# Kernel tuning notes

Hardware: AMD Instinct MI355X
Metric: run time of the kernel (lower is better)

Reference implementation:

```python
import jax, jax.numpy as jnp
import numpy as np

NUM_HEAD = 8
EPS = 1e-12  # matches torch F.normalize default eps


def setup_inputs() -> dict:
    key = jax.random.key(0)
    k1, k2, k3 = jax.random.split(key, 3)
    B, N, C = 8, 8192, 384
    x = jax.random.normal(k1, (B, N, C), dtype=jnp.float32)
    # torch Linear weights: (out_features, in_features)
    w_qkv = jax.random.normal(k2, (3 * C, C), dtype=jnp.float32) * (C ** -0.5)
    w_proj = jax.random.normal(k3, (C, C), dtype=jnp.float32) * (C ** -0.5)
    b_proj = jnp.zeros((C,), dtype=jnp.float32)
    return {"x": x, "w_qkv": w_qkv, "w_proj": w_proj, "b_proj": b_proj}


def _l2norm(t):
    # F.normalize(t, dim=-1): t / max(||t||_2, eps)
    n = jnp.sqrt(jnp.sum(t * t, axis=-1, keepdims=True))
    return t / jnp.maximum(n, EPS)


def reference(x, w_qkv, w_proj, b_proj):
    B, N, C = x.shape
    H = NUM_HEAD
    Dh = C // H
    qkv = x @ w_qkv.T  # (B, N, 3C), qkv_bias=False
    qkv = qkv.reshape(B, N, 3, H, Dh).transpose(2, 0, 3, 1, 4)  # (3, B, H, N, Dh)
    q, k, v = qkv[0], qkv[1], qkv[2]
    # transpose(-2, -1) -> (B, H, Dh, N); normalize along N (cross-covariance attn)
    q = _l2norm(jnp.swapaxes(q, -2, -1))
    k = _l2norm(jnp.swapaxes(k, -2, -1))
    v = jnp.swapaxes(v, -2, -1)  # (B, H, Dh, N)
    attn = jnp.einsum('bhdn,bhen->bhde', q, k)  # (B, H, Dh, Dh)
    attn = jax.nn.softmax(attn, axis=-1)
    out = jnp.einsum('bhde,bhen->bhdn', attn, v)  # (B, H, Dh, N)
    out = out.transpose(0, 3, 1, 2).reshape(B, N, C)  # (B, N, C)
    out = out @ w_proj.T + b_proj
    return out
```

## Files before the change

### kernel.cpp

```cpp
#include <hip/hip_runtime.h>
#include <hip/hip_bf16.h>
#include <stdint.h>


typedef __bf16 bf16_t;
typedef __attribute__((ext_vector_type(8))) __bf16 bf16x8;
typedef __attribute__((ext_vector_type(4))) __bf16 bf16x4;
typedef __attribute__((ext_vector_type(4))) float f32x4;

#define NTOK 8192
#define CDIM 384
#define WH   25165824
#define DHN  393216

#define XCHUNKS 3145728
#define TCHUNKS 3201024

__device__ __forceinline__ f32x4 mfma16(bf16x8 a, bf16x8 b, f32x4 c) {
  return __builtin_amdgcn_mfma_f32_16x16x32_bf16(a, b, c, 0, 0, 0);
}

__device__ __forceinline__ void gload16(bf16_t* lds, const bf16_t* g) {
  __builtin_amdgcn_global_load_lds(
      (const __attribute__((address_space(1))) void*)g,
      (__attribute__((address_space(3))) void*)lds, 16, 0, 0);
}

template <bool BF16>
__device__ __forceinline__ bf16x8 load8(const void* p, int idx) {
  if constexpr (BF16) {
    return *(const bf16x8*)((const bf16_t*)p + idx);
  } else {
    const float* f = (const float*)p + idx;
    f32x4 a = *(const f32x4*)f;
    f32x4 b = *(const f32x4*)(f + 4);
    bf16x8 r;
    r[0] = (bf16_t)a[0]; r[1] = (bf16_t)a[1]; r[2] = (bf16_t)a[2]; r[3] = (bf16_t)a[3];
    r[4] = (bf16_t)b[0]; r[5] = (bf16_t)b[1]; r[6] = (bf16_t)b[2]; r[7] = (bf16_t)b[3];
    return r;
  }
}

__global__ void k_probe(const uint32_t* __restrict__ X, int* __restrict__ flag) {
  __shared__ int cnt;
  if (threadIdx.x == 0) cnt = 0;
  __syncthreads();
  const uint32_t w = X[threadIdx.x];
  const int e = (int)((w >> 7) & 0xFF);
  const int sane = (e >= 110 && e <= 131) ? 1 : 0;
  atomicAdd(&cnt, sane);
  __syncthreads();
  if (threadIdx.x == 0) *flag = (cnt >= 128) ? 1 : 0;
}

__global__ void k_zero(float* __restrict__ p, int n) {
  int i = blockIdx.x * 256 + threadIdx.x;
  if (i < n) p[i] = 0.f;
}

__global__ void k_cvt(const void* __restrict__ X, const void* __restrict__ Wqkv,
                      bf16_t* __restrict__ Xf, bf16_t* __restrict__ Wf,
                      const int* __restrict__ flagp) {
  const int isb = *flagp;
  const int G = gridDim.x * 256;
  for (int c = blockIdx.x * 256 + threadIdx.x; c < TCHUNKS; c += G) {
    const bool isX = c < XCHUNKS;
    const int lc = isX ? c : c - XCHUNKS;
    const int t = lc >> 6, ln = lc & 63;
    const int tm = t / 12, tk = t - tm * 12;
    const int m = tm * 16 + (ln & 15);
    const int k = tk * 32 + ((ln >> 4) << 3);
    const int off = m * CDIM + k;
    const void* src = isX ? X : Wqkv;
    bf16_t* dst = (isX ? Xf : Wf) + (size_t)lc * 8;
    if (isb) {
      *(bf16x8*)dst = *(const bf16x8*)((const bf16_t*)src + off);
    } else {
      const float* f = (const float*)src + off;
      const f32x4 a = *(const f32x4*)f;
      const f32x4 b = *(const f32x4*)(f + 4);
      bf16x8 r;
      r[0] = (bf16_t)a[0]; r[1] = (bf16_t)a[1]; r[2] = (bf16_t)a[2]; r[3] = (bf16_t)a[3];
      r[4] = (bf16_t)b[0]; r[5] = (bf16_t)b[1]; r[6] = (bf16_t)b[2]; r[7] = (bf16_t)b[3];
      *(bf16x8*)dst = r;
    }
  }
}

__global__ __launch_bounds__(256, 3) void k_gemm_qkv(
    const bf16_t* __restrict__ Xf, const bf16_t* __restrict__ Wf,
    bf16_t* __restrict__ qkv) {
  __shared__ __align__(16) bf16_t Bs[24576];

  const int tid = threadIdx.x;
  const int lane = tid & 63;
  const int wv = tid >> 6;
  const int q4 = lane >> 4, l16 = lane & 15;
  const int tok0 = blockIdx.x * 64;
  const int bb = tok0 >> 13;
  const int nB = tok0 & 8191;

  const bf16_t* Bsrc = Xf + (size_t)tok0 * CDIM;
#pragma unroll
  for (int s = 0; s < 12; s++) {
    const int chunk = s * 256 + tid;
    gload16(Bs + chunk * 8, Bsrc + chunk * 8);
  }
  __syncthreads();

  for (int jt = 0; jt < 9; jt++) {
    const int which = jt / 3;
    const int jtt = jt - which * 3;
    f32x4 acc[2][4];
#pragma unroll
    for (int i = 0; i < 2; i++)
#pragma unroll
      for (int j = 0; j < 4; j++) acc[i][j] = (f32x4){0.f, 0.f, 0.f, 0.f};

    const int rt0 = jt * 8 + wv * 2;
#pragma unroll 2
    for (int kc = 0; kc < 12; kc++) {
      bf16x8 af[2], bfr[4];
#pragma unroll
      for (int i = 0; i < 2; i++)
        af[i] = *(const bf16x8*)(Wf + (size_t)((rt0 + i) * 12 + kc) * 512 + lane * 8);
#pragma unroll
      for (int j = 0; j < 4; j++)
        bfr[j] = *(const bf16x8*)&Bs[(j * 12 + kc) * 512 + lane * 8];
      if (which < 2) {
#pragma unroll
        for (int i = 0; i < 2; i++)
#pragma unroll
          for (int j = 0; j < 4; j++) acc[i][j] = mfma16(bfr[j], af[i], acc[i][j]);
      } else {
#pragma unroll
        for (int i = 0; i < 2; i++)
#pragma unroll
          for (int j = 0; j < 4; j++) acc[i][j] = mfma16(af[i], bfr[j], acc[i][j]);
      }
    }

    if (which < 2) {
#pragma unroll
      for (int i = 0; i < 2; i++) {
        const int rin = jtt * 128 + wv * 32 + i * 16 + l16;
        const int h = rin / 48, dh = rin - h * 48;
        bf16_t* rowp = qkv + which * WH + (bb * 8 + h) * DHN + dh * NTOK
                       + nB + q4 * 4;
#pragma unroll
        for (int j = 0; j < 4; j++) {
          bf16x4 o = {(bf16_t)acc[i][j][0], (bf16_t)acc[i][j][1],
                      (bf16_t)acc[i][j][2], (bf16_t)acc[i][j][3]};
          *(bf16x4*)(rowp + j * 16) = o;
        }
      }
    } else {
#pragma unroll
      for (int i = 0; i < 2; i++) {
        const int c0 = jtt * 128 + wv * 32 + i * 16 + q4 * 4;
#pragma unroll
        for (int j = 0; j < 4; j++) {
          const int mg = tok0 + j * 16 + l16;
          bf16x4 o = {(bf16_t)acc[i][j][0], (bf16_t)acc[i][j][1],
                      (bf16_t)acc[i][j][2], (bf16_t)acc[i][j][3]};
          *(bf16x4*)(qkv + 2 * WH + (size_t)mg * CDIM + c0) = o;
        }
      }
    }
  }
}

template <bool BF16>
__device__ __forceinline__ void qkv_body_legacy(const void* __restrict__ X,
                                                const void* __restrict__ Wqkv,
                                                bf16_t* __restrict__ qkv,
                                                bf16_t* As, bf16_t* Bs) {
  const int tid = threadIdx.x;
  const int lane = tid & 63;
  const int wr = tid >> 7, wc = (tid >> 6) & 1;
  const int q4 = lane >> 4, l16 = lane & 15;
  const int rowB0 = blockIdx.x * 128;
  const int r0 = tid >> 2, kk = (tid & 3) << 3;
  const int bb = rowB0 >> 13;
  const int nB = rowB0 & 8191;

  for (int jt = 0; jt < 9; jt++) {
    const int rowA0 = jt * 128;
    const int which = jt / 3;
    const int jtt = jt - which * 3;
    f32x4 acc[4][4];
#pragma unroll
    for (int i = 0; i < 4; i++)
#pragma unroll
      for (int j = 0; j < 4; j++) acc[i][j] = (f32x4){0.f, 0.f, 0.f, 0.f};

    for (int k0 = 0; k0 < CDIM; k0 += 32) {
      bf16x8 a0 = load8<BF16>(Wqkv, (rowA0 + r0) * CDIM + k0 + kk);
      bf16x8 a1 = load8<BF16>(Wqkv, (rowA0 + r0 + 64) * CDIM + k0 + kk);
      bf16x8 b0 = load8<BF16>(X, (rowB0 + r0) * CDIM + k0 + kk);
      bf16x8 b1 = load8<BF16>(X, (rowB0 + r0 + 64) * CDIM + k0 + kk);
      __syncthreads();
      *(bf16x8*)&As[tid * 8] = a0;
      *(bf16x8*)&As[(tid + 256) * 8] = a1;
      *(bf16x8*)&Bs[tid * 8] = b0;
      *(bf16x8*)&Bs[(tid + 256) * 8] = b1;
      __syncthreads();
      bf16x8 af[4], bfr[4];
#pragma unroll
      for (int i = 0; i < 4; i++) {
        af[i]  = *(const bf16x8*)&As[(wr * 64 + i * 16 + l16) * 32 + q4 * 8];
        bfr[i] = *(const bf16x8*)&Bs[(wc * 64 + i * 16 + l16) * 32 + q4 * 8];
      }
      if (which < 2) {
#pragma unroll
        for (int i = 0; i < 4; i++)
#pragma unroll
          for (int j = 0; j < 4; j++) acc[i][j] = mfma16(bfr[j], af[i], acc[i][j]);
      } else {
#pragma unroll
        for (int i = 0; i < 4; i++)
#pragma unroll
          for (int j = 0; j < 4; j++) acc[i][j] = mfma16(af[i], bfr[j], acc[i][j]);
      }
    }

    if (which < 2) {
#pragma unroll
      for (int i = 0; i < 4; i++) {
        const int rin = jtt * 128 + wr * 64 + i * 16 + l16;
        const int h = rin / 48, dh = rin - h * 48;
        bf16_t* rowp = qkv + which * WH + (bb * 8 + h) * DHN + dh * NTOK
                       + nB + wc * 64 + q4 * 4;
#pragma unroll
        for (int j = 0; j < 4; j++) {
          bf16x4 o = {(bf16_t)acc[i][j][0], (bf16_t)acc[i][j][1],
                      (bf16_t)acc[i][j][2], (bf16_t)acc[i][j][3]};
          *(bf16x4*)(rowp + j * 16) = o;
        }
      }
    } else {
#pragma unroll
      for (int i = 0; i < 4; i++) {
        const int rin0 = jtt * 128 + wr * 64 + i * 16 + q4 * 4;
#pragma unroll
        for (int j = 0; j < 4; j++) {
          const int mg = rowB0 + wc * 64 + j * 16 + l16;
          bf16x4 o = {(bf16_t)acc[i][j][0], (bf16_t)acc[i][j][1],
                      (bf16_t)acc[i][j][2], (bf16_t)acc[i][j][3]};
          *(bf16x4*)(qkv + 2 * WH + mg * CDIM + rin0) = o;
        }
      }
    }
  }
}

__global__ __launch_bounds__(256, 2) void k_gemm_qkv_bf16(
    const void* __restrict__ X, const void* __restrict__ Wqkv,
    bf16_t* __restrict__ qkv, const int* __restrict__ flagp) {
  __shared__ __align__(16) bf16_t As[128 * 32];
  __shared__ __align__(16) bf16_t Bs[128 * 32];
  if (!*flagp) return;
  qkv_body_legacy<true>(X, Wqkv, qkv, As, Bs);
}

__global__ __launch_bounds__(256, 2) void k_gemm_qkv_f32(
    const void* __restrict__ X, const void* __restrict__ Wqkv,
    bf16_t* __restrict__ qkv, const int* __restrict__ flagp) {
  __shared__ __align__(16) bf16_t As[128 * 32];
  __shared__ __align__(16) bf16_t Bs[128 * 32];
  if (*flagp) return;
  qkv_body_legacy<false>(X, Wqkv, qkv, As, Bs);
}

__global__ __launch_bounds__(256, 2) void k_gram(
    const bf16_t* __restrict__ qkv, float* __restrict__ S_acc, float* __restrict__ ssq_acc) {
  __shared__ __align__(16) float sm[9312];
  bf16_t* Qs = (bf16_t*)sm;
  bf16_t* Ks = Qs + 6144;
  float* ssq_sm = sm + 9216;

  const int tid = threadIdx.x;
  const int wave = tid >> 6, lane = tid & 63, q4 = lane >> 4, l16 = lane & 15;
  const int s = blockIdx.x, bh = blockIdx.y;
  const bf16_t* Qg = qkv + bh * DHN;
  const bf16_t* Kg = qkv + WH + bh * DHN;

  if (tid < 96) ssq_sm[tid] = 0.f;

  f32x4 acc[3][3];
#pragma unroll
  for (int i = 0; i < 3; i++)
#pragma unroll
    for (int j = 0; j < 3; j++) acc[i][j] = (f32x4){0.f, 0.f, 0.f, 0.f};
  float qss[3] = {0.f, 0.f, 0.f}, kss[3] = {0.f, 0.f, 0.f};

  for (int t0 = 0; t0 < 8; t0++) {
    const int n0 = s * 1024 + t0 * 128;
    bf16x8 qv[3], kv[3];
#pragma unroll
    for (int jj = 0; jj < 3; jj++) {
      const int c = jj * 256 + tid;
      const int st = c / 192, rem = c - st * 192;
      const int row = rem >> 2, kk = (rem & 3) << 3;
      const int gofs = row * NTOK + n0 + st * 32 + kk;
      qv[jj] = *(const bf16x8*)(Qg + gofs);
      kv[jj] = *(const bf16x8*)(Kg + gofs);
    }
    __syncthreads();
#pragma unroll
    for (int jj = 0; jj < 3; jj++) {
      *(bf16x8*)&Qs[(jj * 256 + tid) * 8] = qv[jj];
      *(bf16x8*)&Ks[(jj * 256 + tid) * 8] = kv[jj];
    }
    __syncthreads();
    bf16x8 qf[3], kf[3];
#pragma unroll
    for (int i = 0; i < 3; i++) {
      qf[i] = *(const bf16x8*)&Qs[wave * 1536 + (i * 16 + l16) * 32 + q4 * 8];
      kf[i] = *(const bf16x8*)&Ks[wave * 1536 + (i * 16 + l16) * 32 + q4 * 8];
    }
#pragma unroll
    for (int i = 0; i < 3; i++) {
#pragma unroll
      for (int u = 0; u < 8; u++) {
        const float qv2 = (float)qf[i][u], kv2 = (float)kf[i][u];
        qss[i] += qv2 * qv2;
        kss[i] += kv2 * kv2;
      }
#pragma unroll
      for (int j = 0; j < 3; j++) acc[i][j] = mfma16(qf[i], kf[j], acc[i][j]);
    }
  }

  __syncthreads();
  float* red = sm;
#pragma unroll
  for (int i = 0; i < 3; i++)
#pragma unroll
    for (int j = 0; j < 3; j++)
#pragma unroll
      for (int r = 0; r < 4; r++)
        red[wave * 2304 + (i * 3 + j) * 256 + lane * 4 + r] = acc[i][j][r];
#pragma unroll
  for (int i = 0; i < 3; i++) {
    atomicAdd(&ssq_sm[i * 16 + l16], qss[i]);
    atomicAdd(&ssq_sm[48 + i * 16 + l16], kss[i]);
  }
  __syncthreads();
  for (int idx = tid; idx < 2304; idx += 256) {
    const float v = red[idx] + red[2304 + idx] + red[4608 + idx] + red[6912 + idx];
    const int tile = idx >> 8, ln = (idx >> 2) & 63, r = idx & 3;
    const int i = tile / 3, j = tile - i * 3;
    const int d = i * 16 + ((ln >> 4) << 2) + r;
    const int e = j * 16 + (ln & 15);
    atomicAdd(&S_acc[bh * 2304 + d * 48 + e], v);
  }
  if (tid < 96) atomicAdd(&ssq_acc[bh * 96 + tid], ssq_sm[tid]);
}

__global__ void k_softmax(const float* __restrict__ S_acc, const float* __restrict__ ssq_acc,
                          float* __restrict__ attn_f) {
  __shared__ float invk_sm[48];
  const int bh = blockIdx.x, d = threadIdx.x;
  if (d < 48) invk_sm[d] = 1.f / fmaxf(sqrtf(ssq_acc[bh * 96 + 48 + d]), 1e-12f);
  __syncthreads();
  if (d < 48) {
    const float invq = 1.f / fmaxf(sqrtf(ssq_acc[bh * 96 + d]), 1e-12f);
    float lg[48], mx = -1e30f;
#pragma unroll
    for (int e = 0; e < 48; e++) {
      lg[e] = S_acc[bh * 2304 + d * 48 + e] * invq * invk_sm[e];
      mx = fmaxf(mx, lg[e]);
    }
    float ssum = 0.f;
#pragma unroll
    for (int e = 0; e < 48; e++) { lg[e] = expf(lg[e] - mx); ssum += lg[e]; }
    const float inv = 1.f / ssum;
#pragma unroll
    for (int e = 0; e < 48; e++) attn_f[bh * 2304 + d * 48 + e] = lg[e] * inv;
  }
}

__global__ void k_weff(
    const float* __restrict__ attn_f, const void* __restrict__ Wp,
    bf16_t* __restrict__ Weff, const int* __restrict__ flagp) {
  __shared__ float a_sm[2304];
  __shared__ float w_sm[2304];
  const int isb = *flagp;
  const int bid = blockIdx.x;
  const int ct = bid & 7, h = (bid >> 3) & 7, b = bid >> 6;
  const int bh = b * 8 + h;
  const int tid = threadIdx.x;

  for (int i = tid; i < 2304; i += 256) {
    a_sm[i] = attn_f[bh * 2304 + i];
    const int r = i / 48, c = i - r * 48;
    const int gi = (ct * 48 + r) * CDIM + h * 48 + c;
    w_sm[i] = isb ? (float)((const bf16_t*)Wp)[gi] : ((const float*)Wp)[gi];
  }
  __syncthreads();

  for (int o = tid; o < 2304; o += 256) {
    const int r = o / 48, e = o - r * 48;
    float s = 0.f;
#pragma unroll 8
    for (int d = 0; d < 48; d++) s += w_sm[r * 48 + d] * a_sm[d * 48 + e];
    Weff[b * 147456 + (ct * 48 + r) * CDIM + h * 48 + e] = (bf16_t)s;
  }
}

__global__ __launch_bounds__(256, 2) void k_gemm_out(
    const bf16_t* __restrict__ Weff, const bf16_t* __restrict__ qkv,
    const void* __restrict__ bias, void* __restrict__ out, const int* __restrict__ flagp) {
  __shared__ __align__(16) bf16_t As[2 * 4096];
  __shared__ __align__(16) bf16_t Bs[2 * 4096];
  const int isb = *flagp;
  const int tid = threadIdx.x;
  const int lane = tid & 63;
  const int wr = tid >> 7, wc = (tid >> 6) & 1;
  const int q4 = lane >> 4, l16 = lane & 15;
  const int b = blockIdx.y;
  const int rowB0 = blockIdx.x * 128;
  const bf16_t* Aa = Weff + b * 147456;
  const bf16_t* Ba = qkv + 2 * WH + b * (NTOK * CDIM);
  const int r0 = tid >> 2, kk = (tid & 3) << 3;

  auto STAGE = [&](int cts, int ks, int nxt) {
    const int rowA0 = cts * 128;
    const int k0 = ks * 32;
    bf16_t* Ad = As + nxt * 4096;
    bf16_t* Bd = Bs + nxt * 4096;
    gload16(Ad + tid * 8,         Aa + (rowA0 + r0) * CDIM + k0 + kk);
    gload16(Ad + (tid + 256) * 8, Aa + (rowA0 + r0 + 64) * CDIM + k0 + kk);
    gload16(Bd + tid * 8,         Ba + (rowB0 + r0) * CDIM + k0 + kk);
    gload16(Bd + (tid + 256) * 8, Ba + (rowB0 + r0 + 64) * CDIM + k0 + kk);
  };

  STAGE(0, 0, 0);
  __syncthreads();
  int cur = 0;

  for (int ct = 0; ct < 3; ct++) {
    const int rowA0 = ct * 128;
    f32x4 acc[4][4];
#pragma unroll
    for (int i = 0; i < 4; i++)
#pragma unroll
      for (int j = 0; j < 4; j++) acc[i][j] = (f32x4){0.f, 0.f, 0.f, 0.f};

    for (int k = 0; k < 12; k++) {
      if (!(ct == 2 && k == 11)) {
        int kn = k + 1, cn = ct;
        if (kn == 12) { kn = 0; cn = ct + 1; }
        STAGE(cn, kn, cur ^ 1);
      }
      const bf16_t* Ac = As + cur * 4096;
      const bf16_t* Bc = Bs + cur * 4096;
      bf16x8 af[4], bfr[4];
#pragma unroll
      for (int i = 0; i < 4; i++) {
        af[i]  = *(const bf16x8*)&Ac[(wr * 64 + i * 16 + l16) * 32 + q4 * 8];
        bfr[i] = *(const bf16x8*)&Bc[(wc * 64 + i * 16 + l16) * 32 + q4 * 8];
      }
#pragma unroll
      for (int i = 0; i < 4; i++)
#pragma unroll
        for (int j = 0; j < 4; j++) acc[i][j] = mfma16(af[i], bfr[j], acc[i][j]);
      __syncthreads();
      cur ^= 1;
    }

#pragma unroll
    for (int i = 0; i < 4; i++) {
      const int cg = rowA0 + wr * 64 + i * 16 + q4 * 4;
      float bv[4];
#pragma unroll
      for (int r = 0; r < 4; r++)
        bv[r] = isb ? (float)((const bf16_t*)bias)[cg + r] : ((const float*)bias)[cg + r];
#pragma unroll
      for (int j = 0; j < 4; j++) {
        const int ng = rowB0 + wc * 64 + j * 16 + l16;
        const int oi = (b * NTOK + ng) * CDIM + cg;
        if (isb) {
          bf16x4 o = {(bf16_t)(acc[i][j][0] + bv[0]), (bf16_t)(acc[i][j][1] + bv[1]),
                      (bf16_t)(acc[i][j][2] + bv[2]), (bf16_t)(acc[i][j][3] + bv[3])};
          *(bf16x4*)((bf16_t*)out + oi) = o;
        } else {
          f32x4 o = {acc[i][j][0] + bv[0], acc[i][j][1] + bv[1],
                     acc[i][j][2] + bv[2], acc[i][j][3] + bv[3]};
          *(f32x4*)((float*)out + oi) = o;
        }
      }
    }
  }
}

extern "C" void kernel_launch(void* const* d_in, const int* in_sizes, int n_in,
                              void* d_out, int out_size, void* d_ws, size_t ws_size,
                              hipStream_t stream) {
  (void)in_sizes; (void)n_in; (void)out_size;
  const void* X    = d_in[0];
  const void* Wqkv = d_in[1];
  const void* Wp   = d_in[2];
  const void* bias = d_in[3];

  char* ws = (char*)d_ws;
  bf16_t* qkv    = (bf16_t*)ws;
  float*  S_acc  = (float*)(ws + 150994944);
  float*  ssq    = (float*)(ws + 151584768);
  float*  attn_f = (float*)(ws + 151609344);
  bf16_t* Weff   = (bf16_t*)(ws + 152199168);
  int*    flag   = (int*)(ws + 154558464);
  bf16_t* Xf     = (bf16_t*)(ws + 154558720);
  bf16_t* Wf     = (bf16_t*)(ws + 204890368);

  const bool have_cvt_ws = ws_size >= 205775104ULL;

  k_probe<<<dim3(1), 256, 0, stream>>>((const uint32_t*)X, flag);
  k_zero<<<dim3(600), 256, 0, stream>>>(S_acc, 153600);
  if (have_cvt_ws) {
    k_cvt<<<dim3(2048), 256, 0, stream>>>(X, Wqkv, Xf, Wf, flag);
    k_gemm_qkv<<<dim3(1024), 256, 0, stream>>>(Xf, Wf, qkv);
  } else {
    k_gemm_qkv_bf16<<<dim3(512), 256, 0, stream>>>(X, Wqkv, qkv, flag);
    k_gemm_qkv_f32<<<dim3(512), 256, 0, stream>>>(X, Wqkv, qkv, flag);
  }
  k_gram<<<dim3(8, 64), 256, 0, stream>>>(qkv, S_acc, ssq);
  k_softmax<<<dim3(64), 64, 0, stream>>>(S_acc, ssq, attn_f);
  k_weff<<<dim3(512), 256, 0, stream>>>(attn_f, Wp, Weff, flag);
  k_gemm_out<<<dim3(64, 8), 256, 0, stream>>>(Weff, qkv, bias, d_out, flag);
}
```

Measured before the change: 394.0 us.

## Store Q/K/V and Weff in MFMA-fragment-tiled layout; stream fragments directly

```diff
diff --git a/kernel.cpp b/kernel.cpp
--- a/kernel.cpp
+++ b/kernel.cpp
@@ -87,6 +87,17 @@
   }
 }
 
+__device__ __forceinline__ void store_qk4(bf16_t* plane, int dh, int tok0, bf16x4 o) {
+  const int t = (dh >> 4) * 256 + (tok0 >> 5);
+  const int w = (dh & 15) | (((tok0 >> 3) & 3) << 4);
+  *(bf16x4*)(plane + t * 512 + w * 8 + (tok0 & 7)) = o;
+}
+__device__ __forceinline__ void store_v4(bf16_t* vb, int tok, int c0, bf16x4 o) {
+  const int t = (tok >> 4) * 12 + (c0 >> 5);
+  const int w = (tok & 15) | (((c0 >> 3) & 3) << 4);
+  *(bf16x4*)(vb + t * 512 + w * 8 + (c0 & 7)) = o;
+}
+
 __global__ __launch_bounds__(256, 3) void k_gemm_qkv(
     const bf16_t* __restrict__ Xf, const bf16_t* __restrict__ Wf,
     bf16_t* __restrict__ qkv) {
@@ -108,6 +119,8 @@
   }
   __syncthreads();
 
+  bf16_t* vb = qkv + 2 * WH + (size_t)bb * (NTOK * CDIM);
+
   for (int jt = 0; jt < 9; jt++) {
     const int which = jt / 3;
     const int jtt = jt - which * 3;
@@ -145,13 +158,12 @@
       for (int i = 0; i < 2; i++) {
         const int rin = jtt * 128 + wv * 32 + i * 16 + l16;
         const int h = rin / 48, dh = rin - h * 48;
-        bf16_t* rowp = qkv + which * WH + (bb * 8 + h) * DHN + dh * NTOK
-                       + nB + q4 * 4;
+        bf16_t* plane = qkv + which * WH + (size_t)(bb * 8 + h) * DHN;
 #pragma unroll
         for (int j = 0; j < 4; j++) {
           bf16x4 o = {(bf16_t)acc[i][j][0], (bf16_t)acc[i][j][1],
                       (bf16_t)acc[i][j][2], (bf16_t)acc[i][j][3]};
-          *(bf16x4*)(rowp + j * 16) = o;
+          store_qk4(plane, dh, nB + j * 16 + q4 * 4, o);
         }
       }
     } else {
@@ -160,10 +172,9 @@
         const int c0 = jtt * 128 + wv * 32 + i * 16 + q4 * 4;
 #pragma unroll
         for (int j = 0; j < 4; j++) {
-          const int mg = tok0 + j * 16 + l16;
           bf16x4 o = {(bf16_t)acc[i][j][0], (bf16_t)acc[i][j][1],
                       (bf16_t)acc[i][j][2], (bf16_t)acc[i][j][3]};
-          *(bf16x4*)(qkv + 2 * WH + (size_t)mg * CDIM + c0) = o;
+          store_v4(vb, nB + j * 16 + l16, c0, o);
         }
       }
     }
@@ -183,6 +194,7 @@
   const int r0 = tid >> 2, kk = (tid & 3) << 3;
   const int bb = rowB0 >> 13;
   const int nB = rowB0 & 8191;
+  bf16_t* vb = qkv + 2 * WH + (size_t)bb * (NTOK * CDIM);
 
   for (int jt = 0; jt < 9; jt++) {
     const int rowA0 = jt * 128;
@@ -229,25 +241,23 @@
       for (int i = 0; i < 4; i++) {
         const int rin = jtt * 128 + wr * 64 + i * 16 + l16;
         const int h = rin / 48, dh = rin - h * 48;
-        bf16_t* rowp = qkv + which * WH + (bb * 8 + h) * DHN + dh * NTOK
-                       + nB + wc * 64 + q4 * 4;
+        bf16_t* plane = qkv + which * WH + (size_t)(bb * 8 + h) * DHN;
 #pragma unroll
         for (int j = 0; j < 4; j++) {
           bf16x4 o = {(bf16_t)acc[i][j][0], (bf16_t)acc[i][j][1],
                       (bf16_t)acc[i][j][2], (bf16_t)acc[i][j][3]};
-          *(bf16x4*)(rowp + j * 16) = o;
+          store_qk4(plane, dh, nB + wc * 64 + j * 16 + q4 * 4, o);
         }
       }
     } else {
 #pragma unroll
       for (int i = 0; i < 4; i++) {
-        const int rin0 = jtt * 128 + wr * 64 + i * 16 + q4 * 4;
+        const int c0 = jtt * 128 + wr * 64 + i * 16 + q4 * 4;
 #pragma unroll
         for (int j = 0; j < 4; j++) {
-          const int mg = rowB0 + wc * 64 + j * 16 + l16;
           bf16x4 o = {(bf16_t)acc[i][j][0], (bf16_t)acc[i][j][1],
                       (bf16_t)acc[i][j][2], (bf16_t)acc[i][j][3]};
-          *(bf16x4*)(qkv + 2 * WH + mg * CDIM + rin0) = o;
+          store_v4(vb, nB + wc * 64 + j * 16 + l16, c0, o);
         }
       }
     }
@@ -275,77 +285,64 @@
 __global__ __launch_bounds__(256, 2) void k_gram(
     const bf16_t* __restrict__ qkv, float* __restrict__ S_acc, float* __restrict__ ssq_acc) {
   __shared__ __align__(16) float sm[9312];
-  bf16_t* Qs = (bf16_t*)sm;
-  bf16_t* Ks = Qs + 6144;
   float* ssq_sm = sm + 9216;
 
   const int tid = threadIdx.x;
-  const int wave = tid >> 6, lane = tid & 63, q4 = lane >> 4, l16 = lane & 15;
+  const int wv = tid >> 6, lane = tid & 63, q4 = lane >> 4, l16 = lane & 15;
   const int s = blockIdx.x, bh = blockIdx.y;
-  const bf16_t* Qg = qkv + bh * DHN;
-  const bf16_t* Kg = qkv + WH + bh * DHN;
+  const bf16_t* Qg = qkv + (size_t)bh * DHN;
+  const bf16_t* Kg = qkv + WH + (size_t)bh * DHN;
 
   if (tid < 96) ssq_sm[tid] = 0.f;
-
-  f32x4 acc[3][3];
+  __syncthreads();
+
+  f32x4 acc[3][3], accq[3], acck[3];
+#pragma unroll
+  for (int i = 0; i < 3; i++) {
+    accq[i] = (f32x4){0.f, 0.f, 0.f, 0.f};
+    acck[i] = (f32x4){0.f, 0.f, 0.f, 0.f};
+#pragma unroll
+    for (int j = 0; j < 3; j++) acc[i][j] = (f32x4){0.f, 0.f, 0.f, 0.f};
+  }
+
+  const int tt0 = s * 32 + wv * 8;
+#pragma unroll 2
+  for (int kc = 0; kc < 8; kc++) {
+    const int tt = tt0 + kc;
+    bf16x8 qf[3], kf[3];
+#pragma unroll
+    for (int i = 0; i < 3; i++) {
+      qf[i] = *(const bf16x8*)(Qg + (size_t)(i * 256 + tt) * 512 + lane * 8);
+      kf[i] = *(const bf16x8*)(Kg + (size_t)(i * 256 + tt) * 512 + lane * 8);
+    }
+#pragma unroll
+    for (int i = 0; i < 3; i++) {
+      accq[i] = mfma16(qf[i], qf[i], accq[i]);
+      acck[i] = mfma16(kf[i], kf[i], acck[i]);
+#pragma unroll
+      for (int j = 0; j < 3; j++) acc[i][j] = mfma16(qf[i], kf[j], acc[i][j]);
+    }
+  }
+
+#pragma unroll
+  for (int r = 0; r < 4; r++) {
+    if (l16 == q4 * 4 + r) {
+#pragma unroll
+      for (int i = 0; i < 3; i++) {
+        atomicAdd(&ssq_sm[i * 16 + l16], accq[i][r]);
+        atomicAdd(&ssq_sm[48 + i * 16 + l16], acck[i][r]);
+      }
+    }
+  }
+
+  float* red = sm;
 #pragma unroll
   for (int i = 0; i < 3; i++)
 #pragma unroll
-    for (int j = 0; j < 3; j++) acc[i][j] = (f32x4){0.f, 0.f, 0.f, 0.f};
-  float qss[3] = {0.f, 0.f, 0.f}, kss[3] = {0.f, 0.f, 0.f};
-
-  for (int t0 = 0; t0 < 8; t0++) {
-    const int n0 = s * 1024 + t0 * 128;
-    bf16x8 qv[3], kv[3];
-#pragma unroll
-    for (int jj = 0; jj < 3; jj++) {
-      const int c = jj * 256 + tid;
-      const int st = c / 192, rem = c - st * 192;
-      const int row = rem >> 2, kk = (rem & 3) << 3;
-      const int gofs = row * NTOK + n0 + st * 32 + kk;
-      qv[jj] = *(const bf16x8*)(Qg + gofs);
-      kv[jj] = *(const bf16x8*)(Kg + gofs);
-    }
-    __syncthreads();
-#pragma unroll
-    for (int jj = 0; jj < 3; jj++) {
-      *(bf16x8*)&Qs[(jj * 256 + tid) * 8] = qv[jj];
-      *(bf16x8*)&Ks[(jj * 256 + tid) * 8] = kv[jj];
-    }
-    __syncthreads();
-    bf16x8 qf[3], kf[3];
-#pragma unroll
-    for (int i = 0; i < 3; i++) {
-      qf[i] = *(const bf16x8*)&Qs[wave * 1536 + (i * 16 + l16) * 32 + q4 * 8];
-      kf[i] = *(const bf16x8*)&Ks[wave * 1536 + (i * 16 + l16) * 32 + q4 * 8];
-    }
-#pragma unroll
-    for (int i = 0; i < 3; i++) {
-#pragma unroll
-      for (int u = 0; u < 8; u++) {
-        const float qv2 = (float)qf[i][u], kv2 = (float)kf[i][u];
-        qss[i] += qv2 * qv2;
-        kss[i] += kv2 * kv2;
-      }
-#pragma unroll
-      for (int j = 0; j < 3; j++) acc[i][j] = mfma16(qf[i], kf[j], acc[i][j]);
-    }
-  }
-
-  __syncthreads();
-  float* red = sm;
-#pragma unroll
-  for (int i = 0; i < 3; i++)
-#pragma unroll
     for (int j = 0; j < 3; j++)
 #pragma unroll
       for (int r = 0; r < 4; r++)
-        red[wave * 2304 + (i * 3 + j) * 256 + lane * 4 + r] = acc[i][j][r];
-#pragma unroll
-  for (int i = 0; i < 3; i++) {
-    atomicAdd(&ssq_sm[i * 16 + l16], qss[i]);
-    atomicAdd(&ssq_sm[48 + i * 16 + l16], kss[i]);
-  }
+        red[wv * 2304 + (i * 3 + j) * 256 + lane * 4 + r] = acc[i][j][r];
   __syncthreads();
   for (int idx = tid; idx < 2304; idx += 256) {
     const float v = red[idx] + red[2304 + idx] + red[4608 + idx] + red[6912 + idx];
@@ -400,87 +397,79 @@
   }
   __syncthreads();
 
+  bf16_t* Wb = Weff + (size_t)b * 147456;
   for (int o = tid; o < 2304; o += 256) {
     const int r = o / 48, e = o - r * 48;
     float s = 0.f;
 #pragma unroll 8
     for (int d = 0; d < 48; d++) s += w_sm[r * 48 + d] * a_sm[d * 48 + e];
-    Weff[b * 147456 + (ct * 48 + r) * CDIM + h * 48 + e] = (bf16_t)s;
-  }
-}
-
-__global__ __launch_bounds__(256, 2) void k_gemm_out(
+    const int cp = ct * 48 + r;
+    const int cc = h * 48 + e;
+    const int t = (cp >> 4) * 12 + (cc >> 5);
+    const int w = (cp & 15) | (((cc >> 3) & 3) << 4);
+    Wb[t * 512 + w * 8 + (cc & 7)] = (bf16_t)s;
+  }
+}
+
+__global__ __launch_bounds__(256, 3) void k_gemm_out(
     const bf16_t* __restrict__ Weff, const bf16_t* __restrict__ qkv,
     const void* __restrict__ bias, void* __restrict__ out, const int* __restrict__ flagp) {
-  __shared__ __align__(16) bf16_t As[2 * 4096];
-  __shared__ __align__(16) bf16_t Bs[2 * 4096];
+  __shared__ __align__(16) bf16_t Bs[24576];
+
   const int isb = *flagp;
   const int tid = threadIdx.x;
   const int lane = tid & 63;
-  const int wr = tid >> 7, wc = (tid >> 6) & 1;
+  const int wv = tid >> 6;
   const int q4 = lane >> 4, l16 = lane & 15;
-  const int b = blockIdx.y;
-  const int rowB0 = blockIdx.x * 128;
-  const bf16_t* Aa = Weff + b * 147456;
-  const bf16_t* Ba = qkv + 2 * WH + b * (NTOK * CDIM);
-  const int r0 = tid >> 2, kk = (tid & 3) << 3;
-
-  auto STAGE = [&](int cts, int ks, int nxt) {
-    const int rowA0 = cts * 128;
-    const int k0 = ks * 32;
-    bf16_t* Ad = As + nxt * 4096;
-    bf16_t* Bd = Bs + nxt * 4096;
-    gload16(Ad + tid * 8,         Aa + (rowA0 + r0) * CDIM + k0 + kk);
-    gload16(Ad + (tid + 256) * 8, Aa + (rowA0 + r0 + 64) * CDIM + k0 + kk);
-    gload16(Bd + tid * 8,         Ba + (rowB0 + r0) * CDIM + k0 + kk);
-    gload16(Bd + (tid + 256) * 8, Ba + (rowB0 + r0 + 64) * CDIM + k0 + kk);
-  };
-
-  STAGE(0, 0, 0);
-  __syncthreads();
-  int cur = 0;
+  const int tok0 = blockIdx.x * 64;
+  const int bb = tok0 >> 13;
+  const int nB = tok0 & 8191;
+
+  const bf16_t* Vb = qkv + 2 * WH + (size_t)bb * (NTOK * CDIM);
+  const bf16_t* Af = Weff + (size_t)bb * 147456;
+
+  const bf16_t* Bsrc = Vb + (size_t)nB * CDIM;
+#pragma unroll
+  for (int s = 0; s < 12; s++) {
+    const int chunk = s * 256 + tid;
+    gload16(Bs + chunk * 8, Bsrc + chunk * 8);
+  }
+  __syncthreads();
 
   for (int ct = 0; ct < 3; ct++) {
-    const int rowA0 = ct * 128;
-    f32x4 acc[4][4];
-#pragma unroll
-    for (int i = 0; i < 4; i++)
+    f32x4 acc[2][4];
+#pragma unroll
+    for (int i = 0; i < 2; i++)
 #pragma unroll
       for (int j = 0; j < 4; j++) acc[i][j] = (f32x4){0.f, 0.f, 0.f, 0.f};
 
-    for (int k = 0; k < 12; k++) {
-      if (!(ct == 2 && k == 11)) {
-        int kn = k + 1, cn = ct;
-        if (kn == 12) { kn = 0; cn = ct + 1; }
-        STAGE(cn, kn, cur ^ 1);
-      }
-      const bf16_t* Ac = As + cur * 4096;
-      const bf16_t* Bc = Bs + cur * 4096;
-      bf16x8 af[4], bfr[4];
-#pragma unroll
-      for (int i = 0; i < 4; i++) {
-        af[i]  = *(const bf16x8*)&Ac[(wr * 64 + i * 16 + l16) * 32 + q4 * 8];
-        bfr[i] = *(const bf16x8*)&Bc[(wc * 64 + i * 16 + l16) * 32 + q4 * 8];
-      }
-#pragma unroll
-      for (int i = 0; i < 4; i++)
+    const int rt0 = ct * 8 + wv * 2;
+#pragma unroll 2
+    for (int kc = 0; kc < 12; kc++) {
+      bf16x8 af[2], bfr[4];
+#pragma unroll
+      for (int i = 0; i < 2; i++)
+        af[i] = *(const bf16x8*)(Af + (size_t)((rt0 + i) * 12 + kc) * 512 + lane * 8);
+#pragma unroll
+      for (int j = 0; j < 4; j++)
+        bfr[j] = *(const bf16x8*)&Bs[(j * 12 + kc) * 512 + lane * 8];
+#pragma unroll
+      for (int i = 0; i < 2; i++)
 #pragma unroll
         for (int j = 0; j < 4; j++) acc[i][j] = mfma16(af[i], bfr[j], acc[i][j]);
-      __syncthreads();
-      cur ^= 1;
-    }
-
-#pragma unroll
-    for (int i = 0; i < 4; i++) {
-      const int cg = rowA0 + wr * 64 + i * 16 + q4 * 4;
+    }
+
+#pragma unroll
+    for (int i = 0; i < 2; i++) {
+      const int cg = ct * 128 + wv * 32 + i * 16 + q4 * 4;
       float bv[4];
 #pragma unroll
       for (int r = 0; r < 4; r++)
         bv[r] = isb ? (float)((const bf16_t*)bias)[cg + r] : ((const float*)bias)[cg + r];
 #pragma unroll
       for (int j = 0; j < 4; j++) {
-        const int ng = rowB0 + wc * 64 + j * 16 + l16;
-        const int oi = (b * NTOK + ng) * CDIM + cg;
+        const int tokg = tok0 + j * 16 + l16;
+        const int oi = tokg * CDIM + cg;
         if (isb) {
           bf16x4 o = {(bf16_t)(acc[i][j][0] + bv[0]), (bf16_t)(acc[i][j][1] + bv[1]),
                       (bf16_t)(acc[i][j][2] + bv[2]), (bf16_t)(acc[i][j][3] + bv[3])};
@@ -528,5 +517,5 @@
   k_gram<<<dim3(8, 64), 256, 0, stream>>>(qkv, S_acc, ssq);
   k_softmax<<<dim3(64), 64, 0, stream>>>(S_acc, ssq, attn_f);
   k_weff<<<dim3(512), 256, 0, stream>>>(attn_f, Wp, Weff, flag);
-  k_gemm_out<<<dim3(64, 8), 256, 0, stream>>>(Weff, qkv, bias, d_out, flag);
-}
+  k_gemm_out<<<dim3(1024), 256, 0, stream>>>(Weff, qkv, bias, d_out, flag);
+}
```

Result: no change. 389.8 us (-1.1%).
